# Optimization experiments

Hardware: AMD Instinct MI355X
Metric: run time of the kernel (lower is better)

The kernel has to match this reference:

```python
import jax, jax.numpy as jnp
import numpy as np
from jax import lax

B, S, H, E, F, K = 4, 2048, 1024, 8, 4096, 2

def setup_inputs() -> dict:
    key = jax.random.key(0)
    k1, k2, k3, k4 = jax.random.split(key, 4)
    return {
        "hidden_states": jax.random.normal(k1, (B, S, H), dtype=jnp.float32),
        "router_logits": jax.random.normal(k2, (B, S, E), dtype=jnp.float32),
        "w1": jax.random.normal(k3, (E, H, F), dtype=jnp.float32) * 0.02,
        "w2": jax.random.normal(k4, (E, F, H), dtype=jnp.float32) * 0.02,
        "layer_idx": 0,
    }


def reference(hidden_states, router_logits, w1, w2, layer_idx):
    b, s, h = hidden_states.shape
    e = router_logits.shape[-1]
    T = b * s
    x = hidden_states.reshape(T, h)              # [T, H] flattened tokens
    logits = router_logits.reshape(T, e)          # [T, E]

    # top-k routing, softmax over the selected k scores (as in torch.topk + softmax)
    topk_scores, topk_idx = lax.top_k(logits, K)  # [T, K]
    probs = jax.nn.softmax(topk_scores, axis=-1)  # [T, K]

    # scatter combine weights into a dense [T, E] map (dispatch weights)
    cw = jnp.zeros((T, e), dtype=probs.dtype).at[jnp.arange(T)[:, None], topk_idx].add(probs)

    # grouped expert compute: scan over experts, masked weighted accumulation
    def step(acc, ew):
        w1e, w2e, ce = ew                          # [H,F], [F,H], [T]
        he = jax.nn.gelu(x @ w1e) @ w2e            # [T, H] expert FFN
        return acc + ce[:, None] * he, None

    out, _ = lax.scan(step, jnp.zeros_like(x), (w1, w2, cw.T))
    return out.reshape(b, s, h)
```

## Files before the change

kernel.cpp:

```cpp
#include <hip/hip_runtime.h>

#define T_TOKENS 8192
#define H_DIM 1024
#define E_EXP 8
#define F_DIM 4096
#define CAP 8192
#define MT_TILES 32

typedef __attribute__((ext_vector_type(8))) short short8;
typedef __attribute__((ext_vector_type(8))) unsigned short ushort8;
typedef __attribute__((ext_vector_type(4))) float f32x4;

__device__ __forceinline__ unsigned short f2bf(float f) {
    unsigned int u = __float_as_uint(f);
    u += 0x7fffu + ((u >> 16) & 1u);
    return (unsigned short)(u >> 16);
}

__device__ __forceinline__ float gelu_tanh(float x) {
    float z = 0.7978845608028654f * (x + 0.044715f * x * x * x);
    float t = 1.0f - 2.0f / (__expf(2.0f * z) + 1.0f);
    return 0.5f * x * (1.0f + t);
}

__device__ __forceinline__ void gld16(const void* g, void* l) {
    __builtin_amdgcn_global_load_lds(
        (const __attribute__((address_space(1))) unsigned int*)g,
        (__attribute__((address_space(3))) unsigned int*)l,
        16, 0, 0);
}

__global__ void router_kernel(const float* __restrict__ logits,
                              int* __restrict__ cnt,
                              int* __restrict__ tok,
                              float* __restrict__ wt) {
    __shared__ int hcnt[E_EXP];
    __shared__ int hbase[E_EXP];
    int tid = threadIdx.x;
    if (tid < E_EXP) hcnt[tid] = 0;
    __syncthreads();
    int t = blockIdx.x * 256 + tid;
    float l[E_EXP];
#pragma unroll
    for (int i = 0; i < E_EXP; i++) l[i] = logits[t * E_EXP + i];
    int i0 = 0; float s0 = l[0];
#pragma unroll
    for (int i = 1; i < E_EXP; i++) if (l[i] > s0) { s0 = l[i]; i0 = i; }
    int i1 = (i0 == 0) ? 1 : 0; float s1 = l[i1];
#pragma unroll
    for (int i = 0; i < E_EXP; i++) if (i != i0 && l[i] > s1) { s1 = l[i]; i1 = i; }
    float p0 = 1.0f / (1.0f + __expf(s1 - s0));
    float p1 = 1.0f - p0;
    int lo0 = atomicAdd(&hcnt[i0], 1);
    int lo1 = atomicAdd(&hcnt[i1], 1);
    __syncthreads();
    if (tid < E_EXP) hbase[tid] = atomicAdd(&cnt[tid], hcnt[tid]);
    __syncthreads();
    int sl0 = hbase[i0] + lo0;
    tok[i0 * CAP + sl0] = t; wt[i0 * CAP + sl0] = p0;
    int sl1 = hbase[i1] + lo1;
    tok[i1 * CAP + sl1] = t; wt[i1 * CAP + sl1] = p1;
}

__global__ void base_kernel(const int* __restrict__ cnt, int* __restrict__ base) {
    if (threadIdx.x == 0) {
        int b = 0;
        for (int e = 0; e < E_EXP; e++) { base[e] = b; b += cnt[e]; }
    }
}

__global__ void cvtx_kernel(const float* __restrict__ x, unsigned short* __restrict__ xg) {
    int i = blockIdx.x * 256 + threadIdx.x;
    float4 v = ((const float4*)x)[i];
    ushort4 o;
    o.x = f2bf(v.x); o.y = f2bf(v.y); o.z = f2bf(v.z); o.w = f2bf(v.w);
    ((ushort4*)xg)[i] = o;
}

__global__ void tcvt_kernel(const float* __restrict__ in, unsigned short* __restrict__ out,
                            int M, int N) {
    __shared__ float t[64][65];
    size_t eoff = (size_t)blockIdx.z * M * N;
    in += eoff; out += eoff;
    int r0 = blockIdx.x * 64, c0 = blockIdx.y * 64;
    int tid = threadIdx.x;
    int srow = tid >> 4;
    int scol = (tid & 15) * 4;
#pragma unroll
    for (int p = 0; p < 4; p++) {
        int row = p * 16 + srow;
        float4 v = *(const float4*)&in[(size_t)(r0 + row) * N + c0 + scol];
        t[row][scol + 0] = v.x; t[row][scol + 1] = v.y;
        t[row][scol + 2] = v.z; t[row][scol + 3] = v.w;
    }
    __syncthreads();
    int orow = tid >> 3;
    int ocb = (tid & 7) * 8;
#pragma unroll
    for (int p = 0; p < 2; p++) {
        int r = p * 32 + orow;
        ushort8 o;
#pragma unroll
        for (int i = 0; i < 8; i++) o[i] = f2bf(t[ocb + i][r]);
        *(ushort8*)&out[(size_t)(c0 + r) * M + r0 + ocb] = o;
    }
}

template <int GATHER, int EPI, int NT8, int MC>
__global__ __launch_bounds__(256, 4)
void gemm_kernel(const unsigned short* __restrict__ Asrc,
                 const unsigned short* __restrict__ Bt,
                 int K, int N,
                 const int* __restrict__ cnt, const int* __restrict__ base,
                 const int* __restrict__ tok, const float* __restrict__ wt,
                 unsigned short* __restrict__ Gout, float* __restrict__ out) {
    int bid = blockIdx.x;
    int xcd = bid & 7;
    int q = bid >> 3;
    int nl = q % NT8;
    int q2 = q / NT8;
    const int MTG = MT_TILES / MC;
    int mt = q2 % MTG;
    const int e = q2 / MTG;
    const int g = xcd & (MC - 1);
    const int n_tile = (xcd / MC) * NT8 + nl;
    const int m_tile = mt * MC + g;

    const int cnt_e = cnt[e];
    const int m0 = m_tile * 128;
    if (m0 >= cnt_e) return;
    const int base_e = base[e];
    const int n0 = n_tile * 128;
    const int tid = threadIdx.x;
    const int lane = tid & 63;
    const int wave = tid >> 6;
    const int quad = lane >> 4, l16 = lane & 15;
    const int wm = (wave & 1) * 64, wn = (wave >> 1) * 64;

    __shared__ unsigned short As[2][128][32];
    __shared__ unsigned short Bs[2][128][32];

    const int srow = wave * 16 + (lane >> 2);
    const int selem = (lane & 3) * 8;
    const unsigned short* aptr[2];
    const unsigned short* bptr[2];
#pragma unroll
    for (int p = 0; p < 2; p++) {
        int gr = m0 + p * 64 + srow;
        if (gr > cnt_e - 1) gr = cnt_e - 1;
        const unsigned short* arow;
        if (GATHER) arow = Asrc + (size_t)tok[e * CAP + gr] * K;
        else        arow = Asrc + (size_t)(base_e + gr) * K;
        aptr[p] = arow + selem;
        bptr[p] = Bt + (size_t)e * (size_t)N * K + (size_t)(n0 + p * 64 + srow) * K + selem;
    }
    unsigned short* alds0 = &As[0][wave * 16][0];
    unsigned short* alds1 = &As[0][64 + wave * 16][0];
    unsigned short* blds0 = &Bs[0][wave * 16][0];
    unsigned short* blds1 = &Bs[0][64 + wave * 16][0];
    const int HALF = 128 * 32;

    f32x4 acc[4][4];
#pragma unroll
    for (int i = 0; i < 4; i++)
#pragma unroll
        for (int j = 0; j < 4; j++) acc[i][j] = (f32x4){0.f, 0.f, 0.f, 0.f};

    for (int k0 = 0; k0 < K; k0 += 64) {
#pragma unroll
        for (int sub = 0; sub < 2; sub++) {
            gld16(aptr[0] + k0 + sub * 32, alds0 + sub * HALF);
            gld16(aptr[1] + k0 + sub * 32, alds1 + sub * HALF);
            gld16(bptr[0] + k0 + sub * 32, blds0 + sub * HALF);
            gld16(bptr[1] + k0 + sub * 32, blds1 + sub * HALF);
        }
        __syncthreads();
#pragma unroll
        for (int sub = 0; sub < 2; sub++) {
            short8 af[4], bf[4];
#pragma unroll
            for (int i = 0; i < 4; i++)
                af[i] = *(const short8*)&As[sub][wm + i * 16 + l16][quad * 8];
#pragma unroll
            for (int j = 0; j < 4; j++)
                bf[j] = *(const short8*)&Bs[sub][wn + j * 16 + l16][quad * 8];
#pragma unroll
            for (int i = 0; i < 4; i++)
#pragma unroll
                for (int j = 0; j < 4; j++)
                    acc[i][j] = __builtin_amdgcn_mfma_f32_16x16x32_bf16(af[i], bf[j], acc[i][j], 0, 0, 0);
        }
        __syncthreads();
    }

    if (EPI == 0) {
#pragma unroll
        for (int i = 0; i < 4; i++) {
            int lm = wm + i * 16 + quad * 4;
#pragma unroll
            for (int r = 0; r < 4; r++) {
                int gr = m0 + lm + r;
                if (gr < cnt_e) {
                    size_t rowoff = (size_t)(base_e + gr) * N;
#pragma unroll
                    for (int j = 0; j < 4; j++) {
                        int ncol = n0 + wn + j * 16 + l16;
                        Gout[rowoff + ncol] = f2bf(gelu_tanh(acc[i][j][r]));
                    }
                }
            }
        }
    } else {
#pragma unroll
        for (int i = 0; i < 4; i++) {
            int lm = wm + i * 16 + quad * 4;
#pragma unroll
            for (int r = 0; r < 4; r++) {
                int gr = m0 + lm + r;
                if (gr < cnt_e) {
                    int tk = tok[e * CAP + gr];
                    float w = wt[e * CAP + gr];
                    float* orow = out + (size_t)tk * N;
#pragma unroll
                    for (int j = 0; j < 4; j++) {
                        int ncol = n0 + wn + j * 16 + l16;
                        atomicAdd(&orow[ncol], w * acc[i][j][r]);
                    }
                }
            }
        }
    }
}

extern "C" void kernel_launch(void* const* d_in, const int* in_sizes, int n_in,
                              void* d_out, int out_size, void* d_ws, size_t ws_size,
                              hipStream_t stream) {
    const float* x      = (const float*)d_in[0];
    const float* logits = (const float*)d_in[1];
    const float* w1     = (const float*)d_in[2];
    const float* w2     = (const float*)d_in[3];
    float* out = (float*)d_out;
    char* ws = (char*)d_ws;

    const size_t OFF_CNT  = 0;
    const size_t OFF_BASE = 64;
    const size_t OFF_TOK  = 1024;
    const size_t OFF_WT   = OFF_TOK + (size_t)E_EXP * CAP * 4;
    const size_t OFF_XG   = 1u << 20;
    const size_t OFF_W1T  = OFF_XG + (size_t)T_TOKENS * H_DIM * 2;
    const size_t OFF_W2T  = OFF_W1T + (size_t)E_EXP * H_DIM * F_DIM * 2;
    const size_t OFF_G    = OFF_W2T + (size_t)E_EXP * H_DIM * F_DIM * 2;

    int* cnt  = (int*)(ws + OFF_CNT);
    int* base = (int*)(ws + OFF_BASE);
    int* tok  = (int*)(ws + OFF_TOK);
    float* wt = (float*)(ws + OFF_WT);
    unsigned short* xg  = (unsigned short*)(ws + OFF_XG);
    unsigned short* w1t = (unsigned short*)(ws + OFF_W1T);
    unsigned short* w2t = (unsigned short*)(ws + OFF_W2T);
    unsigned short* G   = (unsigned short*)(ws + OFF_G);

    hipMemsetAsync(d_out, 0, (size_t)out_size * sizeof(float), stream);
    hipMemsetAsync(cnt, 0, 64, stream);

    router_kernel<<<T_TOKENS / 256, 256, 0, stream>>>(logits, cnt, tok, wt);
    base_kernel<<<1, 64, 0, stream>>>(cnt, base);
    cvtx_kernel<<<(T_TOKENS * H_DIM / 4) / 256, 256, 0, stream>>>(x, xg);
    tcvt_kernel<<<dim3(H_DIM / 64, F_DIM / 64, E_EXP), 256, 0, stream>>>(w1, w1t, H_DIM, F_DIM);
    tcvt_kernel<<<dim3(F_DIM / 64, H_DIM / 64, E_EXP), 256, 0, stream>>>(w2, w2t, F_DIM, H_DIM);
    gemm_kernel<1, 0, 4, 1><<<8 * 4 * MT_TILES * E_EXP, 256, 0, stream>>>(
        xg, w1t, H_DIM, F_DIM, cnt, base, tok, wt, G, nullptr);
    gemm_kernel<0, 1, 2, 2><<<8 * 2 * (MT_TILES / 2) * E_EXP, 256, 0, stream>>>(
        G, w2t, F_DIM, H_DIM, cnt, base, tok, wt, nullptr, out);
    (void)in_sizes; (void)n_in; (void)ws_size;
}
```

Baseline: 749.2 us.

## Use 256x256 tiles with double-buffered swizzled LDS and split-K for second GEMM

Replaces the 128x128 grouped GEMM with a 512-thread 256x256 tile kernel that double-buffers LDS and prefetches the next K slice while computing the current one. The LDS layout gets an XOR swizzle to avoid bank conflicts, and setprio is raised around the MFMA blocks. The down-projection uses split-K by 2 with atomic accumulation, which the existing atomic epilogue already supports. The aim is more data reuse per tile and overlap of loads with compute, at the cost of higher register and LDS use, lower occupancy, and wasted work in partially filled 256-row tiles.

Result: slower. 898.0 us (+19.9%).

```diff
diff --git a/kernel.cpp b/kernel.cpp
--- a/kernel.cpp
+++ b/kernel.cpp
@@ -5,7 +5,7 @@
 #define E_EXP 8
 #define F_DIM 4096
 #define CAP 8192
-#define MT_TILES 32
+#define MT256 16
 
 typedef __attribute__((ext_vector_type(8))) short short8;
 typedef __attribute__((ext_vector_type(8))) unsigned short ushort8;
@@ -106,97 +106,124 @@
     }
 }
 
-template <int GATHER, int EPI, int NT8, int MC>
-__global__ __launch_bounds__(256, 4)
-void gemm_kernel(const unsigned short* __restrict__ Asrc,
-                 const unsigned short* __restrict__ Bt,
-                 int K, int N,
-                 const int* __restrict__ cnt, const int* __restrict__ base,
-                 const int* __restrict__ tok, const float* __restrict__ wt,
-                 unsigned short* __restrict__ Gout, float* __restrict__ out) {
+template <int GATHER, int EPI, int NT, int KSPLIT>
+__global__ __launch_bounds__(512, 2)
+void gemm256_kernel(const unsigned short* __restrict__ Asrc,
+                    const unsigned short* __restrict__ Bt,
+                    int K, int N,
+                    const int* __restrict__ cnt, const int* __restrict__ base,
+                    const int* __restrict__ tok, const float* __restrict__ wt,
+                    unsigned short* __restrict__ Gout, float* __restrict__ out) {
+    const int nwg = E_EXP * MT256 * NT * KSPLIT;
     int bid = blockIdx.x;
-    int xcd = bid & 7;
-    int q = bid >> 3;
-    int nl = q % NT8;
-    int q2 = q / NT8;
-    const int MTG = MT_TILES / MC;
-    int mt = q2 % MTG;
-    const int e = q2 / MTG;
-    const int g = xcd & (MC - 1);
-    const int n_tile = (xcd / MC) * NT8 + nl;
-    const int m_tile = mt * MC + g;
+    int swz = (bid & 7) * (nwg >> 3) + (bid >> 3);
+    const int mt = swz & (MT256 - 1);
+    int rest = swz >> 4;
+    const int ks = rest % KSPLIT; rest /= KSPLIT;
+    const int nt = rest % NT;
+    const int e  = rest / NT;
 
     const int cnt_e = cnt[e];
-    const int m0 = m_tile * 128;
+    const int m0 = mt * 256;
     if (m0 >= cnt_e) return;
     const int base_e = base[e];
-    const int n0 = n_tile * 128;
+    const int n0 = nt * 256;
+    const int Kp = K / KSPLIT;
+    const int kbegin = ks * Kp;
+    const int KT = Kp >> 6;
+
     const int tid = threadIdx.x;
     const int lane = tid & 63;
     const int wave = tid >> 6;
-    const int quad = lane >> 4, l16 = lane & 15;
-    const int wm = (wave & 1) * 64, wn = (wave >> 1) * 64;
-
-    __shared__ unsigned short As[2][128][32];
-    __shared__ unsigned short Bs[2][128][32];
-
-    const int srow = wave * 16 + (lane >> 2);
-    const int selem = (lane & 3) * 8;
-    const unsigned short* aptr[2];
-    const unsigned short* bptr[2];
-#pragma unroll
-    for (int p = 0; p < 2; p++) {
-        int gr = m0 + p * 64 + srow;
+    const int l16 = lane & 15, quad = lane >> 4;
+    const int wmg = wave >> 2;
+    const int wng = wave & 3;
+
+    __shared__ unsigned short As[2][2][128][64];
+    __shared__ unsigned short Bs[2][2][128][64];
+
+    const int rsel = tid >> 3, csel = tid & 7;
+    const int swzc = (csel ^ (rsel & 7)) * 8;
+    const unsigned short* arow[4];
+    const unsigned short* brow[4];
+#pragma unroll
+    for (int ii = 0; ii < 4; ii++) {
+        int gr = m0 + ii * 64 + rsel;
         if (gr > cnt_e - 1) gr = cnt_e - 1;
-        const unsigned short* arow;
-        if (GATHER) arow = Asrc + (size_t)tok[e * CAP + gr] * K;
-        else        arow = Asrc + (size_t)(base_e + gr) * K;
-        aptr[p] = arow + selem;
-        bptr[p] = Bt + (size_t)e * (size_t)N * K + (size_t)(n0 + p * 64 + srow) * K + selem;
-    }
-    unsigned short* alds0 = &As[0][wave * 16][0];
-    unsigned short* alds1 = &As[0][64 + wave * 16][0];
-    unsigned short* blds0 = &Bs[0][wave * 16][0];
-    unsigned short* blds1 = &Bs[0][64 + wave * 16][0];
-    const int HALF = 128 * 32;
-
-    f32x4 acc[4][4];
-#pragma unroll
-    for (int i = 0; i < 4; i++)
+        const unsigned short* ab;
+        if (GATHER) ab = Asrc + (size_t)tok[e * CAP + gr] * K;
+        else        ab = Asrc + (size_t)(base_e + gr) * K;
+        arow[ii] = ab + kbegin + swzc;
+        brow[ii] = Bt + (size_t)e * N * K + (size_t)(n0 + ii * 64 + rsel) * K + kbegin + swzc;
+    }
+    unsigned short* alds = &As[0][0][0][0];
+    unsigned short* blds = &Bs[0][0][0][0];
+    const int dstoff = tid * 8;
+    const int BUFS = 2 * 128 * 64;
+
+    auto stage = [&](int b, int koff) {
+#pragma unroll
+        for (int ii = 0; ii < 4; ii++)
+            gld16(arow[ii] + koff, alds + b * BUFS + ii * 4096 + dstoff);
+#pragma unroll
+        for (int ii = 0; ii < 4; ii++)
+            gld16(brow[ii] + koff, blds + b * BUFS + ii * 4096 + dstoff);
+    };
+
+    f32x4 acc[8][4];
+#pragma unroll
+    for (int i = 0; i < 8; i++)
 #pragma unroll
         for (int j = 0; j < 4; j++) acc[i][j] = (f32x4){0.f, 0.f, 0.f, 0.f};
 
-    for (int k0 = 0; k0 < K; k0 += 64) {
-#pragma unroll
-        for (int sub = 0; sub < 2; sub++) {
-            gld16(aptr[0] + k0 + sub * 32, alds0 + sub * HALF);
-            gld16(aptr[1] + k0 + sub * 32, alds1 + sub * HALF);
-            gld16(bptr[0] + k0 + sub * 32, blds0 + sub * HALF);
-            gld16(bptr[1] + k0 + sub * 32, blds1 + sub * HALF);
-        }
-        __syncthreads();
-#pragma unroll
-        for (int sub = 0; sub < 2; sub++) {
-            short8 af[4], bf[4];
+    const int kx0 = ((quad    ) ^ (l16 & 7)) * 8;
+    const int kx1 = ((quad + 4) ^ (l16 & 7)) * 8;
+
+    stage(0, 0);
+    int koff = 64;
+    for (int t = 0; t < KT; ++t) {
+        const int cur = t & 1;
+        if (t + 1 < KT) {
+            stage(cur ^ 1, koff);
+            asm volatile("s_waitcnt vmcnt(8)\n\ts_barrier" ::: "memory");
+        } else {
+            asm volatile("s_waitcnt vmcnt(0)\n\ts_barrier" ::: "memory");
+        }
+
+        short8 bfr[2][4];
+#pragma unroll
+        for (int j = 0; j < 4; j++) {
+            bfr[0][j] = *(const short8*)&Bs[cur][wng >> 1][(wng & 1) * 64 + j * 16 + l16][kx0];
+            bfr[1][j] = *(const short8*)&Bs[cur][wng >> 1][(wng & 1) * 64 + j * 16 + l16][kx1];
+        }
+#pragma unroll
+        for (int ms = 0; ms < 2; ms++) {
+            short8 afr[2][4];
+#pragma unroll
+            for (int i = 0; i < 4; i++) {
+                afr[0][i] = *(const short8*)&As[cur][wmg][(ms * 4 + i) * 16 + l16][kx0];
+                afr[1][i] = *(const short8*)&As[cur][wmg][(ms * 4 + i) * 16 + l16][kx1];
+            }
+            __builtin_amdgcn_s_setprio(1);
 #pragma unroll
             for (int i = 0; i < 4; i++)
-                af[i] = *(const short8*)&As[sub][wm + i * 16 + l16][quad * 8];
-#pragma unroll
-            for (int j = 0; j < 4; j++)
-                bf[j] = *(const short8*)&Bs[sub][wn + j * 16 + l16][quad * 8];
-#pragma unroll
-            for (int i = 0; i < 4; i++)
-#pragma unroll
-                for (int j = 0; j < 4; j++)
-                    acc[i][j] = __builtin_amdgcn_mfma_f32_16x16x32_bf16(af[i], bf[j], acc[i][j], 0, 0, 0);
-        }
-        __syncthreads();
+#pragma unroll
+                for (int j = 0; j < 4; j++) {
+                    acc[ms * 4 + i][j] = __builtin_amdgcn_mfma_f32_16x16x32_bf16(
+                        afr[0][i], bfr[0][j], acc[ms * 4 + i][j], 0, 0, 0);
+                    acc[ms * 4 + i][j] = __builtin_amdgcn_mfma_f32_16x16x32_bf16(
+                        afr[1][i], bfr[1][j], acc[ms * 4 + i][j], 0, 0, 0);
+                }
+            __builtin_amdgcn_s_setprio(0);
+        }
+        asm volatile("s_barrier" ::: "memory");
+        koff += 64;
     }
 
     if (EPI == 0) {
 #pragma unroll
-        for (int i = 0; i < 4; i++) {
-            int lm = wm + i * 16 + quad * 4;
+        for (int i = 0; i < 8; i++) {
+            int lm = wmg * 128 + i * 16 + quad * 4;
 #pragma unroll
             for (int r = 0; r < 4; r++) {
                 int gr = m0 + lm + r;
@@ -204,7 +231,7 @@
                     size_t rowoff = (size_t)(base_e + gr) * N;
 #pragma unroll
                     for (int j = 0; j < 4; j++) {
-                        int ncol = n0 + wn + j * 16 + l16;
+                        int ncol = n0 + wng * 64 + j * 16 + l16;
                         Gout[rowoff + ncol] = f2bf(gelu_tanh(acc[i][j][r]));
                     }
                 }
@@ -212,8 +239,8 @@
         }
     } else {
 #pragma unroll
-        for (int i = 0; i < 4; i++) {
-            int lm = wm + i * 16 + quad * 4;
+        for (int i = 0; i < 8; i++) {
+            int lm = wmg * 128 + i * 16 + quad * 4;
 #pragma unroll
             for (int r = 0; r < 4; r++) {
                 int gr = m0 + lm + r;
@@ -223,7 +250,7 @@
                     float* orow = out + (size_t)tk * N;
 #pragma unroll
                     for (int j = 0; j < 4; j++) {
-                        int ncol = n0 + wn + j * 16 + l16;
+                        int ncol = n0 + wng * 64 + j * 16 + l16;
                         atomicAdd(&orow[ncol], w * acc[i][j][r]);
                     }
                 }
@@ -268,9 +295,9 @@
     cvtx_kernel<<<(T_TOKENS * H_DIM / 4) / 256, 256, 0, stream>>>(x, xg);
     tcvt_kernel<<<dim3(H_DIM / 64, F_DIM / 64, E_EXP), 256, 0, stream>>>(w1, w1t, H_DIM, F_DIM);
     tcvt_kernel<<<dim3(F_DIM / 64, H_DIM / 64, E_EXP), 256, 0, stream>>>(w2, w2t, F_DIM, H_DIM);
-    gemm_kernel<1, 0, 4, 1><<<8 * 4 * MT_TILES * E_EXP, 256, 0, stream>>>(
+    gemm256_kernel<1, 0, 16, 1><<<E_EXP * MT256 * 16 * 1, 512, 0, stream>>>(
         xg, w1t, H_DIM, F_DIM, cnt, base, tok, wt, G, nullptr);
-    gemm_kernel<0, 1, 2, 2><<<8 * 2 * (MT_TILES / 2) * E_EXP, 256, 0, stream>>>(
+    gemm256_kernel<0, 1, 4, 2><<<E_EXP * MT256 * 4 * 2, 512, 0, stream>>>(
         G, w2t, F_DIM, H_DIM, cnt, base, tok, wt, nullptr, out);
     (void)in_sizes; (void)n_in; (void)ws_size;
 }
```
